# Optimization experiments

Hardware: AMD Instinct MI355X
Metric: run time of the kernel (lower is better)

## Reference

```python
import jax, jax.numpy as jnp
import numpy as np

SINKHORN_ITERS = 100
SINKHORN_EPS = 0.1


def setup_inputs() -> dict:
    key = jax.random.key(0)
    k1, k2 = jax.random.split(key)
    M, N, C = 2048, 2048, 512
    d_M_q = jax.random.normal(k1, (M, C), dtype=jnp.float32)
    d_N_r = jax.random.normal(k2, (N, C), dtype=jnp.float32)
    # pipeline feeds L2-normalized descriptors (F.normalize(..., p=2, dim=1))
    d_M_q = d_M_q / jnp.linalg.norm(d_M_q, axis=1, keepdims=True)
    d_N_r = d_N_r / jnp.linalg.norm(d_N_r, axis=1, keepdims=True)
    z = jnp.float32(0.5)  # learned bin_score scalar
    return {"d_M_q": d_M_q, "d_N_r": d_N_r, "z": z}


def reference(d_M_q, d_N_r, z):
    M, N = d_M_q.shape[0], d_N_r.shape[0]
    # score matmul: (M, C) x (C, N) -> (M, N)
    score = jnp.einsum('mc,nc->mn', d_M_q, d_N_r)
    # augmented (M+1, N+1): dustbin row/col/corner filled with z
    S_aug = jnp.full((M + 1, N + 1), z, dtype=d_M_q.dtype).at[:M, :N].set(score)
    K0 = jnp.exp(S_aug / SINKHORN_EPS)

    def body(i, K):
        K = K / K.sum(axis=1, keepdims=True)  # row normalize
        K = K / K.sum(axis=0, keepdims=True)  # col normalize
        return K

    P_aug = jax.lax.fori_loop(0, SINKHORN_ITERS, body, K0)
    P = P_aug[:M, :N]
    return P, P_aug
```

## Files before the change

### kernel.cpp

```cpp
#include <hip/hip_runtime.h>
#include <hip/hip_fp16.h>

#define ITERS 100
#define AGENT __HIP_MEMORY_SCOPE_AGENT

union PK { unsigned long long u; struct { float v; unsigned tag; } s; };

#define SLOT 136
#define MSG_ONE (2 * 16 * 16 * SLOT)
#define UV_STRIDE 272

__device__ __forceinline__ float wave_sum(float p) {
    p += __shfl_xor(p, 1, 64);
    p += __shfl_xor(p, 2, 64);
    p += __shfl_xor(p, 4, 64);
    p += __shfl_xor(p, 8, 64);
    p += __shfl_xor(p, 16, 64);
    p += __shfl_xor(p, 32, 64);
    return p;
}

__global__ void __launch_bounds__(256, 1)
sinkhorn_fused(const float* __restrict__ Q, const float* __restrict__ R,
               const float* __restrict__ zp, float* __restrict__ out,
               unsigned long long* __restrict__ ws)
{
    __shared__ __align__(16) char smem[66560];
    float* As = (float*)smem;
    float* Bs = (float*)(smem + 32768);
    char*  TrmB = smem;
    char*  TcmB = smem + 32768;
    float* part = (float*)(smem + 65536);

    const int t  = threadIdx.x;
    const int b  = blockIdx.x;
    const int bi = b >> 4, bj = b & 15;
    const int tx = t & 15, ty = t >> 4;
    const int l  = t & 63, w  = t >> 6;
    const int gi0 = bi * 128, gj0 = bj * 128;

    float acc[8][8];
#pragma unroll
    for (int r = 0; r < 8; r++)
#pragma unroll
        for (int c = 0; c < 8; c++) acc[r][c] = 0.f;

    const int lr = t & 31, lc4 = t >> 5;
    const float* Qb = Q + (size_t)gi0 * 512;
    const float* Rb = R + (size_t)gj0 * 512;

    float4 qa[4], ra[4];
#pragma unroll
    for (int i = 0; i < 4; i++) {
        qa[i] = *(const float4*)(Qb + (size_t)(lr + 32 * i) * 512 + 4 * lc4);
        ra[i] = *(const float4*)(Rb + (size_t)(lr + 32 * i) * 512 + 4 * lc4);
    }
#pragma unroll
    for (int i = 0; i < 4; i++) {
        int row = lr + 32 * i;
        As[(4*lc4+0)*128 + row] = qa[i].x;  As[(4*lc4+1)*128 + row] = qa[i].y;
        As[(4*lc4+2)*128 + row] = qa[i].z;  As[(4*lc4+3)*128 + row] = qa[i].w;
        Bs[(4*lc4+0)*128 + row] = ra[i].x;  Bs[(4*lc4+1)*128 + row] = ra[i].y;
        Bs[(4*lc4+2)*128 + row] = ra[i].z;  Bs[(4*lc4+3)*128 + row] = ra[i].w;
    }
    __syncthreads();

    for (int ks = 0; ks < 16; ks++) {
        if (ks < 15) {
            int k0 = (ks + 1) * 32;
#pragma unroll
            for (int i = 0; i < 4; i++) {
                qa[i] = *(const float4*)(Qb + (size_t)(lr+32*i)*512 + k0 + 4*lc4);
                ra[i] = *(const float4*)(Rb + (size_t)(lr+32*i)*512 + k0 + 4*lc4);
            }
        }
        const float* A = As + (ks & 1) * (32 * 128);
        const float* B = Bs + (ks & 1) * (32 * 128);
#pragma unroll 4
        for (int k = 0; k < 32; k++) {
            float4 a0 = *(const float4*)(A + k*128 + 8*ty);
            float4 a1 = *(const float4*)(A + k*128 + 8*ty + 4);
            float4 b0 = *(const float4*)(B + k*128 + 8*tx);
            float4 b1 = *(const float4*)(B + k*128 + 8*tx + 4);
            float av[8] = {a0.x,a0.y,a0.z,a0.w,a1.x,a1.y,a1.z,a1.w};
            float bv[8] = {b0.x,b0.y,b0.z,b0.w,b1.x,b1.y,b1.z,b1.w};
#pragma unroll
            for (int r = 0; r < 8; r++)
#pragma unroll
                for (int c = 0; c < 8; c++)
                    acc[r][c] = fmaf(av[r], bv[c], acc[r][c]);
        }
        if (ks < 15) {
            __syncthreads();
            float* An = As + ((ks+1) & 1) * (32 * 128);
            float* Bn = Bs + ((ks+1) & 1) * (32 * 128);
#pragma unroll
            for (int i = 0; i < 4; i++) {
                int row = lr + 32 * i;
                An[(4*lc4+0)*128 + row] = qa[i].x;  An[(4*lc4+1)*128 + row] = qa[i].y;
                An[(4*lc4+2)*128 + row] = qa[i].z;  An[(4*lc4+3)*128 + row] = qa[i].w;
                Bn[(4*lc4+0)*128 + row] = ra[i].x;  Bn[(4*lc4+1)*128 + row] = ra[i].y;
                Bn[(4*lc4+2)*128 + row] = ra[i].z;  Bn[(4*lc4+3)*128 + row] = ra[i].w;
            }
            __syncthreads();
        }
    }
    __syncthreads();

    const float E = expf(zp[0] * 10.0f);
#pragma unroll
    for (int r = 0; r < 8; r++)
#pragma unroll
        for (int c = 0; c < 8; c++) acc[r][c] = expf(acc[r][c] * 10.0f);

#pragma unroll
    for (int r = 0; r < 8; r++) {
        int rr = 8 * ty + r;
        unsigned short h[8];
#pragma unroll
        for (int c = 0; c < 8; c++) h[c] = __half_as_ushort(__float2half(acc[r][c]));
        uint4 pk;
        pk.x = h[0] | ((unsigned)h[1] << 16); pk.y = h[2] | ((unsigned)h[3] << 16);
        pk.z = h[4] | ((unsigned)h[5] << 16); pk.w = h[6] | ((unsigned)h[7] << 16);
        *(uint4*)(TrmB + rr * 256 + ((tx ^ (rr & 15)) << 4)) = pk;
    }
#pragma unroll
    for (int c = 0; c < 8; c++) {
        int cc = 8 * tx + c;
        unsigned short h[8];
#pragma unroll
        for (int r = 0; r < 8; r++) h[r] = __half_as_ushort(__float2half(acc[r][c]));
        uint4 pk;
        pk.x = h[0] | ((unsigned)h[1] << 16); pk.y = h[2] | ((unsigned)h[3] << 16);
        pk.z = h[4] | ((unsigned)h[5] << 16); pk.w = h[6] | ((unsigned)h[7] << 16);
        *(uint4*)(TcmB + cc * 256 + ((ty ^ (cc & 15)) << 4)) = pk;
    }

    unsigned long long* rmsg = ws;
    unsigned long long* cmsg = ws + MSG_ONE;
    float* uvb  = (float*)(ws + 2 * MSG_ONE) + b * UV_STRIDE;
    float* ubuf = uvb;
    float* vbuf = uvb + 136;

    if (t < 128)      vbuf[t] = 1.0f;
    else if (t < 130) vbuf[t] = 64.0f;
    float uN = 0.f, vN = 1.0f, vsum = 128.0f, usum = 0.f;
    __syncthreads();

    for (int it = 0; it < ITERS; it++) {
        const int buf = it & 1;
        const unsigned tagw = (unsigned)(it + 1);

        {
            unsigned long long* base = rmsg + (size_t)((buf * 16 + bi) * 16) * SLOT;
            if (t == 128) {
                PK p; p.s.v = vsum; p.s.tag = tagw;
                __hip_atomic_store(base + (size_t)bj * SLOT + 128, p.u, __ATOMIC_RELAXED, AGENT);
            }
            if (t < 128) {
                const char* rp = TrmB + t * 256;
                const float4* v4 = (const float4*)vbuf;
                float racc = 0.f;
#pragma unroll
                for (int c = 0; c < 16; c++) {
                    uint4 kq = *(const uint4*)(rp + ((c ^ (t & 15)) << 4));
                    float4 va = v4[2 * c], vb = v4[2 * c + 1];
                    const __half2* h2 = (const __half2*)&kq;
                    float2 f;
                    f = __half22float2(h2[0]); racc = fmaf(f.x, va.x, fmaf(f.y, va.y, racc));
                    f = __half22float2(h2[1]); racc = fmaf(f.x, va.z, fmaf(f.y, va.w, racc));
                    f = __half22float2(h2[2]); racc = fmaf(f.x, vb.x, fmaf(f.y, vb.y, racc));
                    f = __half22float2(h2[3]); racc = fmaf(f.x, vb.z, fmaf(f.y, vb.w, racc));
                }
                PK p; p.s.v = racc; p.s.tag = tagw;
                __hip_atomic_store(base + (size_t)bj * SLOT + t, p.u, __ATOMIC_RELAXED, AGENT);
            }
            float ssum_v = 0.f;
            {
                const int row  = t & 127;
                const int half = t >> 7;
                bool sdone = (half == 1) || (l >= 16);
                float vsv = 0.f, pacc = 0.f;
                unsigned long long* rb = base + (size_t)(8 * half) * SLOT + row;
                for (;;) {
                    PK m[8];
#pragma unroll
                    for (int s = 0; s < 8; s++)
                        m[s].u = __hip_atomic_load(rb + (size_t)s * SLOT,
                                                   __ATOMIC_RELAXED, AGENT);
                    PK vm; vm.u = 0ull;
                    if (!sdone)
                        vm.u = __hip_atomic_load(base + (size_t)l * SLOT + 128,
                                                 __ATOMIC_RELAXED, AGENT);
                    int cnt = 0; float a = 0.f;
#pragma unroll
                    for (int s = 0; s < 8; s++) {
                        bool ok = (m[s].s.tag == tagw);
                        cnt += ok; a += ok ? m[s].s.v : 0.f;
                    }
                    if (!sdone && vm.s.tag == tagw) { vsv = vm.s.v; sdone = true; }
                    if (cnt == 8 && sdone) { pacc = a; break; }
                    __builtin_amdgcn_s_sleep(1);
                }
                part[t] = pacc;
                ssum_v = wave_sum(l < 16 ? vsv : 0.f);
            }
            __syncthreads();
            if (t < 128) {
                float rsum = part[t] + part[t + 128];
                uN = 1.0f / (E * (ssum_v + vN));
                float ui = 1.0f / (rsum + E * vN);
                ubuf[t] = ui;
                float wsm = wave_sum(ui);
                if (l == 0) ubuf[128 + w] = wsm;
            }
            __syncthreads();
            usum = ubuf[128] + ubuf[129];
        }

        {
            unsigned long long* base = cmsg + (size_t)((buf * 16 + bj) * 16) * SLOT;
            if (t == 128) {
                PK p; p.s.v = usum; p.s.tag = tagw;
                __hip_atomic_store(base + (size_t)bi * SLOT + 128, p.u, __ATOMIC_RELAXED, AGENT);
            }
            if (t < 128) {
                const char* cp = TcmB + t * 256;
                const float4* u4 = (const float4*)ubuf;
                float cacc = 0.f;
#pragma unroll
                for (int c = 0; c < 16; c++) {
                    uint4 kq = *(const uint4*)(cp + ((c ^ (t & 15)) << 4));
                    float4 ua = u4[2 * c], ub = u4[2 * c + 1];
                    const __half2* h2 = (const __half2*)&kq;
                    float2 f;
                    f = __half22float2(h2[0]); cacc = fmaf(f.x, ua.x, fmaf(f.y, ua.y, cacc));
                    f = __half22float2(h2[1]); cacc = fmaf(f.x, ua.z, fmaf(f.y, ua.w, cacc));
                    f = __half22float2(h2[2]); cacc = fmaf(f.x, ub.x, fmaf(f.y, ub.y, cacc));
                    f = __half22float2(h2[3]); cacc = fmaf(f.x, ub.z, fmaf(f.y, ub.w, cacc));
                }
                PK p; p.s.v = cacc; p.s.tag = tagw;
                __hip_atomic_store(base + (size_t)bi * SLOT + t, p.u, __ATOMIC_RELAXED, AGENT);
            }
            float ssum_u = 0.f;
            {
                const int row  = t & 127;
                const int half = t >> 7;
                bool sdone = (l >= 16);
                float usv = 0.f, pacc = 0.f;
                unsigned long long* rb = base + (size_t)(8 * half) * SLOT + row;
                for (;;) {
                    PK m[8];
#pragma unroll
                    for (int s = 0; s < 8; s++)
                        m[s].u = __hip_atomic_load(rb + (size_t)s * SLOT,
                                                   __ATOMIC_RELAXED, AGENT);
                    PK um; um.u = 0ull;
                    if (!sdone)
                        um.u = __hip_atomic_load(base + (size_t)l * SLOT + 128,
                                                 __ATOMIC_RELAXED, AGENT);
                    int cnt = 0; float a = 0.f;
#pragma unroll
                    for (int s = 0; s < 8; s++) {
                        bool ok = (m[s].s.tag == tagw);
                        cnt += ok; a += ok ? m[s].s.v : 0.f;
                    }
                    if (!sdone && um.s.tag == tagw) { usv = um.s.v; sdone = true; }
                    if (cnt == 8 && sdone) { pacc = a; break; }
                    __builtin_amdgcn_s_sleep(1);
                }
                part[t] = pacc;
                ssum_u = wave_sum(l < 16 ? usv : 0.f);
            }
            vN = 1.0f / (E * (ssum_u + uN));
            __syncthreads();
            if (t < 128) {
                float csum = part[t] + part[t + 128];
                float vj = 1.0f / (csum + E * uN);
                vbuf[t] = vj;
                float wsm = wave_sum(vj);
                if (l == 0) vbuf[128 + w] = wsm;
            }
            __syncthreads();
            vsum = vbuf[128] + vbuf[129];
        }
    }

    float* P  = out;
    float* PA = out + (size_t)2048 * 2048;
    float2 vv = *(const float2*)&vbuf[2 * l];
#pragma unroll 2
    for (int rr2 = 0; rr2 < 32; rr2++) {
        int i = 32 * w + rr2;
        float ui = ubuf[i];
        const char* rp = TrmB + i * 256;
        int c = l >> 2;
        __half2 h2 = *(const __half2*)(rp + ((c ^ (i & 15)) << 4) + (l & 3) * 4);
        float2 kf = __half22float2(h2);
        float p0 = ui * kf.x * vv.x;
        float p1 = ui * kf.y * vv.y;
        size_t gi = (size_t)(gi0 + i);
        *(float2*)&P[gi * 2048 + gj0 + 2 * l] = make_float2(p0, p1);
        PA[gi * 2049 + gj0 + 2 * l]     = p0;
        PA[gi * 2049 + gj0 + 2 * l + 1] = p1;
        if (bj == 15 && l == 0) PA[gi * 2049 + 2048] = ui * E * vN;
    }
    if (bi == 15 && w == 0) {
        PA[(size_t)2048 * 2049 + gj0 + 2 * l]     = uN * E * vv.x;
        PA[(size_t)2048 * 2049 + gj0 + 2 * l + 1] = uN * E * vv.y;
        if (bj == 15 && l == 0) PA[(size_t)2048 * 2049 + 2048] = uN * E * vN;
    }
}

extern "C" void kernel_launch(void* const* d_in, const int* in_sizes, int n_in,
                              void* d_out, int out_size, void* d_ws, size_t ws_size,
                              hipStream_t stream)
{
    (void)in_sizes; (void)n_in; (void)out_size; (void)ws_size;
    const float* Q  = (const float*)d_in[0];
    const float* R  = (const float*)d_in[1];
    const float* zp = (const float*)d_in[2];
    float* out = (float*)d_out;
    unsigned long long* ws = (unsigned long long*)d_ws;
    void* args[] = { (void*)&Q, (void*)&R, (void*)&zp, (void*)&out, (void*)&ws };
    hipLaunchCooperativeKernel((const void*)sinkhorn_fused, dim3(256), dim3(256),
                               args, 0, stream);
}
```

Baseline: 847.4 us.

## Repartition Sinkhorn kernel into row/column strips with global scaling-vector exchange

```diff
diff --git a/kernel.cpp b/kernel.cpp
--- a/kernel.cpp
+++ b/kernel.cpp
@@ -5,10 +5,6 @@
 #define AGENT __HIP_MEMORY_SCOPE_AGENT
 
 union PK { unsigned long long u; struct { float v; unsigned tag; } s; };
-
-#define SLOT 136
-#define MSG_ONE (2 * 16 * 16 * SLOT)
-#define UV_STRIDE 272
 
 __device__ __forceinline__ float wave_sum(float p) {
     p += __shfl_xor(p, 1, 64);
@@ -25,291 +21,232 @@
                const float* __restrict__ zp, float* __restrict__ out,
                unsigned long long* __restrict__ ws)
 {
-    __shared__ __align__(16) char smem[66560];
-    float* As = (float*)smem;
-    float* Bs = (float*)(smem + 32768);
-    char*  TrmB = smem;
-    char*  TcmB = smem + 32768;
-    float* part = (float*)(smem + 65536);
-
-    const int t  = threadIdx.x;
-    const int b  = blockIdx.x;
-    const int bi = b >> 4, bj = b & 15;
-    const int tx = t & 15, ty = t >> 4;
-    const int l  = t & 63, w  = t >> 6;
-    const int gi0 = bi * 128, gj0 = bj * 128;
-
-    float acc[8][8];
-#pragma unroll
-    for (int r = 0; r < 8; r++)
-#pragma unroll
-        for (int c = 0; c < 8; c++) acc[r][c] = 0.f;
-
-    const int lr = t & 31, lc4 = t >> 5;
-    const float* Qb = Q + (size_t)gi0 * 512;
-    const float* Rb = R + (size_t)gj0 * 512;
-
-    float4 qa[4], ra[4];
-#pragma unroll
-    for (int i = 0; i < 4; i++) {
-        qa[i] = *(const float4*)(Qb + (size_t)(lr + 32 * i) * 512 + 4 * lc4);
-        ra[i] = *(const float4*)(Rb + (size_t)(lr + 32 * i) * 512 + 4 * lc4);
-    }
-#pragma unroll
-    for (int i = 0; i < 4; i++) {
-        int row = lr + 32 * i;
-        As[(4*lc4+0)*128 + row] = qa[i].x;  As[(4*lc4+1)*128 + row] = qa[i].y;
-        As[(4*lc4+2)*128 + row] = qa[i].z;  As[(4*lc4+3)*128 + row] = qa[i].w;
-        Bs[(4*lc4+0)*128 + row] = ra[i].x;  Bs[(4*lc4+1)*128 + row] = ra[i].y;
-        Bs[(4*lc4+2)*128 + row] = ra[i].z;  Bs[(4*lc4+3)*128 + row] = ra[i].w;
-    }
+    __shared__ __align__(16) char smem[66048];
+    char* KrowB = smem;
+    char* KcolB = smem + 32768;
+    float* red  = (float*)(smem + 65536);
+    float* red2 = (float*)(smem + 65664);
+    float* uown = (float*)(smem + 65680);
+    float* vown = (float*)(smem + 65712);
+
+    const int t = threadIdx.x;
+    const int b = blockIdx.x;
+    const int l = t & 63, w = t >> 6;
+    const float E = expf(zp[0] * 10.0f);
+
+    {
+        float acc[8][8];
+#pragma unroll
+        for (int r = 0; r < 8; r++)
+#pragma unroll
+            for (int c = 0; c < 8; c++) acc[r][c] = 0.f;
+        const float* Qs = Q + (size_t)(8 * b) * 512;
+        const float* Rt = R + (size_t)(8 * t) * 512;
+        for (int k = 0; k < 512; k += 4) {
+            float4 r4[8];
+#pragma unroll
+            for (int c = 0; c < 8; c++) r4[c] = *(const float4*)(Rt + c * 512 + k);
+#pragma unroll
+            for (int r = 0; r < 8; r++) {
+                float4 q = *(const float4*)(Qs + r * 512 + k);
+#pragma unroll
+                for (int c = 0; c < 8; c++)
+                    acc[r][c] = fmaf(q.x, r4[c].x, fmaf(q.y, r4[c].y,
+                                fmaf(q.z, r4[c].z, fmaf(q.w, r4[c].w, acc[r][c]))));
+            }
+        }
+#pragma unroll
+        for (int r = 0; r < 8; r++) {
+            unsigned short h[8];
+#pragma unroll
+            for (int c = 0; c < 8; c++)
+                h[c] = __half_as_ushort(__float2half(expf(acc[r][c] * 10.0f)));
+            uint4 pk;
+            pk.x = h[0] | ((unsigned)h[1] << 16); pk.y = h[2] | ((unsigned)h[3] << 16);
+            pk.z = h[4] | ((unsigned)h[5] << 16); pk.w = h[6] | ((unsigned)h[7] << 16);
+            *(uint4*)(KrowB + r * 4096 + t * 16) = pk;
+        }
+    }
+    {
+        float acc[8][8];
+#pragma unroll
+        for (int c = 0; c < 8; c++)
+#pragma unroll
+            for (int i = 0; i < 8; i++) acc[c][i] = 0.f;
+        const float* Rs = R + (size_t)(8 * b) * 512;
+        const float* Qt = Q + (size_t)(8 * t) * 512;
+        for (int k = 0; k < 512; k += 4) {
+            float4 q4[8];
+#pragma unroll
+            for (int i = 0; i < 8; i++) q4[i] = *(const float4*)(Qt + i * 512 + k);
+#pragma unroll
+            for (int c = 0; c < 8; c++) {
+                float4 r = *(const float4*)(Rs + c * 512 + k);
+#pragma unroll
+                for (int i = 0; i < 8; i++)
+                    acc[c][i] = fmaf(r.x, q4[i].x, fmaf(r.y, q4[i].y,
+                                fmaf(r.z, q4[i].z, fmaf(r.w, q4[i].w, acc[c][i]))));
+            }
+        }
+#pragma unroll
+        for (int c = 0; c < 8; c++) {
+            unsigned short h[8];
+#pragma unroll
+            for (int i = 0; i < 8; i++)
+                h[i] = __half_as_ushort(__float2half(expf(acc[c][i] * 10.0f)));
+            uint4 pk;
+            pk.x = h[0] | ((unsigned)h[1] << 16); pk.y = h[2] | ((unsigned)h[3] << 16);
+            pk.z = h[4] | ((unsigned)h[5] << 16); pk.w = h[6] | ((unsigned)h[7] << 16);
+            *(uint4*)(KcolB + c * 4096 + t * 16) = pk;
+        }
+    }
+
+    unsigned long long* umsg = ws;
+    unsigned long long* vmsg = ws + 2 * 2048;
+
+    float v[8], ug[8];
+#pragma unroll
+    for (int c = 0; c < 8; c++) v[c] = 1.0f;
+    float vN = 1.0f, uN = 0.0f, sv = 2048.0f, su = 0.0f;
     __syncthreads();
 
-    for (int ks = 0; ks < 16; ks++) {
-        if (ks < 15) {
-            int k0 = (ks + 1) * 32;
-#pragma unroll
-            for (int i = 0; i < 4; i++) {
-                qa[i] = *(const float4*)(Qb + (size_t)(lr+32*i)*512 + k0 + 4*lc4);
-                ra[i] = *(const float4*)(Rb + (size_t)(lr+32*i)*512 + k0 + 4*lc4);
-            }
-        }
-        const float* A = As + (ks & 1) * (32 * 128);
-        const float* B = Bs + (ks & 1) * (32 * 128);
-#pragma unroll 4
-        for (int k = 0; k < 32; k++) {
-            float4 a0 = *(const float4*)(A + k*128 + 8*ty);
-            float4 a1 = *(const float4*)(A + k*128 + 8*ty + 4);
-            float4 b0 = *(const float4*)(B + k*128 + 8*tx);
-            float4 b1 = *(const float4*)(B + k*128 + 8*tx + 4);
-            float av[8] = {a0.x,a0.y,a0.z,a0.w,a1.x,a1.y,a1.z,a1.w};
-            float bv[8] = {b0.x,b0.y,b0.z,b0.w,b1.x,b1.y,b1.z,b1.w};
-#pragma unroll
-            for (int r = 0; r < 8; r++)
-#pragma unroll
-                for (int c = 0; c < 8; c++)
-                    acc[r][c] = fmaf(av[r], bv[c], acc[r][c]);
-        }
-        if (ks < 15) {
-            __syncthreads();
-            float* An = As + ((ks+1) & 1) * (32 * 128);
-            float* Bn = Bs + ((ks+1) & 1) * (32 * 128);
-#pragma unroll
-            for (int i = 0; i < 4; i++) {
-                int row = lr + 32 * i;
-                An[(4*lc4+0)*128 + row] = qa[i].x;  An[(4*lc4+1)*128 + row] = qa[i].y;
-                An[(4*lc4+2)*128 + row] = qa[i].z;  An[(4*lc4+3)*128 + row] = qa[i].w;
-                Bn[(4*lc4+0)*128 + row] = ra[i].x;  Bn[(4*lc4+1)*128 + row] = ra[i].y;
-                Bn[(4*lc4+2)*128 + row] = ra[i].z;  Bn[(4*lc4+3)*128 + row] = ra[i].w;
-            }
-            __syncthreads();
-        }
-    }
-    __syncthreads();
-
-    const float E = expf(zp[0] * 10.0f);
-#pragma unroll
-    for (int r = 0; r < 8; r++)
-#pragma unroll
-        for (int c = 0; c < 8; c++) acc[r][c] = expf(acc[r][c] * 10.0f);
-
-#pragma unroll
-    for (int r = 0; r < 8; r++) {
-        int rr = 8 * ty + r;
-        unsigned short h[8];
-#pragma unroll
-        for (int c = 0; c < 8; c++) h[c] = __half_as_ushort(__float2half(acc[r][c]));
-        uint4 pk;
-        pk.x = h[0] | ((unsigned)h[1] << 16); pk.y = h[2] | ((unsigned)h[3] << 16);
-        pk.z = h[4] | ((unsigned)h[5] << 16); pk.w = h[6] | ((unsigned)h[7] << 16);
-        *(uint4*)(TrmB + rr * 256 + ((tx ^ (rr & 15)) << 4)) = pk;
-    }
-#pragma unroll
-    for (int c = 0; c < 8; c++) {
-        int cc = 8 * tx + c;
-        unsigned short h[8];
-#pragma unroll
-        for (int r = 0; r < 8; r++) h[r] = __half_as_ushort(__float2half(acc[r][c]));
-        uint4 pk;
-        pk.x = h[0] | ((unsigned)h[1] << 16); pk.y = h[2] | ((unsigned)h[3] << 16);
-        pk.z = h[4] | ((unsigned)h[5] << 16); pk.w = h[6] | ((unsigned)h[7] << 16);
-        *(uint4*)(TcmB + cc * 256 + ((ty ^ (cc & 15)) << 4)) = pk;
-    }
-
-    unsigned long long* rmsg = ws;
-    unsigned long long* cmsg = ws + MSG_ONE;
-    float* uvb  = (float*)(ws + 2 * MSG_ONE) + b * UV_STRIDE;
-    float* ubuf = uvb;
-    float* vbuf = uvb + 136;
-
-    if (t < 128)      vbuf[t] = 1.0f;
-    else if (t < 130) vbuf[t] = 64.0f;
-    float uN = 0.f, vN = 1.0f, vsum = 128.0f, usum = 0.f;
-    __syncthreads();
-
     for (int it = 0; it < ITERS; it++) {
+        const unsigned tagw = (unsigned)(it + 1);
         const int buf = it & 1;
-        const unsigned tagw = (unsigned)(it + 1);
 
         {
-            unsigned long long* base = rmsg + (size_t)((buf * 16 + bi) * 16) * SLOT;
-            if (t == 128) {
-                PK p; p.s.v = vsum; p.s.tag = tagw;
-                __hip_atomic_store(base + (size_t)bj * SLOT + 128, p.u, __ATOMIC_RELAXED, AGENT);
-            }
-            if (t < 128) {
-                const char* rp = TrmB + t * 256;
-                const float4* v4 = (const float4*)vbuf;
-                float racc = 0.f;
-#pragma unroll
-                for (int c = 0; c < 16; c++) {
-                    uint4 kq = *(const uint4*)(rp + ((c ^ (t & 15)) << 4));
-                    float4 va = v4[2 * c], vb = v4[2 * c + 1];
-                    const __half2* h2 = (const __half2*)&kq;
-                    float2 f;
-                    f = __half22float2(h2[0]); racc = fmaf(f.x, va.x, fmaf(f.y, va.y, racc));
-                    f = __half22float2(h2[1]); racc = fmaf(f.x, va.z, fmaf(f.y, va.w, racc));
-                    f = __half22float2(h2[2]); racc = fmaf(f.x, vb.x, fmaf(f.y, vb.y, racc));
-                    f = __half22float2(h2[3]); racc = fmaf(f.x, vb.z, fmaf(f.y, vb.w, racc));
+            float p[8];
+#pragma unroll
+            for (int r = 0; r < 8; r++) p[r] = 0.f;
+#pragma unroll
+            for (int r = 0; r < 8; r++) {
+                uint4 kq = *(const uint4*)(KrowB + r * 4096 + t * 16);
+                const __half2* h2 = (const __half2*)&kq;
+                float2 f;
+                f = __half22float2(h2[0]); p[r] = fmaf(f.x, v[0], fmaf(f.y, v[1], p[r]));
+                f = __half22float2(h2[1]); p[r] = fmaf(f.x, v[2], fmaf(f.y, v[3], p[r]));
+                f = __half22float2(h2[2]); p[r] = fmaf(f.x, v[4], fmaf(f.y, v[5], p[r]));
+                f = __half22float2(h2[3]); p[r] = fmaf(f.x, v[6], fmaf(f.y, v[7], p[r]));
+            }
+#pragma unroll
+            for (int r = 0; r < 8; r++) p[r] = wave_sum(p[r]);
+            if (l == 0) {
+#pragma unroll
+                for (int r = 0; r < 8; r++) red[w * 8 + r] = p[r];
+            }
+            uN = 1.0f / (E * (sv + vN));
+            __syncthreads();
+            if (t < 8) {
+                float rsum = red[t] + red[8 + t] + red[16 + t] + red[24 + t];
+                float uu = 1.0f / (rsum + E * vN);
+                uown[t] = uu;
+                PK pk; pk.s.v = uu; pk.s.tag = tagw;
+                __hip_atomic_store(umsg + (size_t)buf * 2048 + 8 * b + t, pk.u,
+                                   __ATOMIC_RELAXED, AGENT);
+            }
+            unsigned long long* gb = umsg + (size_t)buf * 2048 + 8 * t;
+            for (;;) {
+                PK m[8];
+#pragma unroll
+                for (int s = 0; s < 8; s++)
+                    m[s].u = __hip_atomic_load(gb + s, __ATOMIC_RELAXED, AGENT);
+                int cnt = 0;
+#pragma unroll
+                for (int s = 0; s < 8; s++) cnt += (m[s].s.tag == tagw);
+                if (cnt == 8) {
+#pragma unroll
+                    for (int s = 0; s < 8; s++) ug[s] = m[s].s.v;
+                    break;
                 }
-                PK p; p.s.v = racc; p.s.tag = tagw;
-                __hip_atomic_store(base + (size_t)bj * SLOT + t, p.u, __ATOMIC_RELAXED, AGENT);
-            }
-            float ssum_v = 0.f;
-            {
-                const int row  = t & 127;
-                const int half = t >> 7;
-                bool sdone = (half == 1) || (l >= 16);
-                float vsv = 0.f, pacc = 0.f;
-                unsigned long long* rb = base + (size_t)(8 * half) * SLOT + row;
-                for (;;) {
-                    PK m[8];
-#pragma unroll
-                    for (int s = 0; s < 8; s++)
-                        m[s].u = __hip_atomic_load(rb + (size_t)s * SLOT,
-                                                   __ATOMIC_RELAXED, AGENT);
-                    PK vm; vm.u = 0ull;
-                    if (!sdone)
-                        vm.u = __hip_atomic_load(base + (size_t)l * SLOT + 128,
-                                                 __ATOMIC_RELAXED, AGENT);
-                    int cnt = 0; float a = 0.f;
-#pragma unroll
-                    for (int s = 0; s < 8; s++) {
-                        bool ok = (m[s].s.tag == tagw);
-                        cnt += ok; a += ok ? m[s].s.v : 0.f;
-                    }
-                    if (!sdone && vm.s.tag == tagw) { vsv = vm.s.v; sdone = true; }
-                    if (cnt == 8 && sdone) { pacc = a; break; }
-                    __builtin_amdgcn_s_sleep(1);
+                __builtin_amdgcn_s_sleep(1);
+            }
+            float sp = ug[0] + ug[1] + ug[2] + ug[3] + ug[4] + ug[5] + ug[6] + ug[7];
+            sp = wave_sum(sp);
+            if (l == 0) red2[w] = sp;
+            __syncthreads();
+            su = red2[0] + red2[1] + red2[2] + red2[3];
+        }
+
+        {
+            float p[8];
+#pragma unroll
+            for (int c = 0; c < 8; c++) p[c] = 0.f;
+#pragma unroll
+            for (int c = 0; c < 8; c++) {
+                uint4 kq = *(const uint4*)(KcolB + c * 4096 + t * 16);
+                const __half2* h2 = (const __half2*)&kq;
+                float2 f;
+                f = __half22float2(h2[0]); p[c] = fmaf(f.x, ug[0], fmaf(f.y, ug[1], p[c]));
+                f = __half22float2(h2[1]); p[c] = fmaf(f.x, ug[2], fmaf(f.y, ug[3], p[c]));
+                f = __half22float2(h2[2]); p[c] = fmaf(f.x, ug[4], fmaf(f.y, ug[5], p[c]));
+                f = __half22float2(h2[3]); p[c] = fmaf(f.x, ug[6], fmaf(f.y, ug[7], p[c]));
+            }
+#pragma unroll
+            for (int c = 0; c < 8; c++) p[c] = wave_sum(p[c]);
+            if (l == 0) {
+#pragma unroll
+                for (int c = 0; c < 8; c++) red[w * 8 + c] = p[c];
+            }
+            const float vNn = 1.0f / (E * (su + uN));
+            __syncthreads();
+            if (t < 8) {
+                float csum = red[t] + red[8 + t] + red[16 + t] + red[24 + t];
+                float vv = 1.0f / (csum + E * uN);
+                vown[t] = vv;
+                PK pk; pk.s.v = vv; pk.s.tag = tagw;
+                __hip_atomic_store(vmsg + (size_t)buf * 2048 + 8 * b + t, pk.u,
+                                   __ATOMIC_RELAXED, AGENT);
+            }
+            unsigned long long* gb = vmsg + (size_t)buf * 2048 + 8 * t;
+            for (;;) {
+                PK m[8];
+#pragma unroll
+                for (int s = 0; s < 8; s++)
+                    m[s].u = __hip_atomic_load(gb + s, __ATOMIC_RELAXED, AGENT);
+                int cnt = 0;
+#pragma unroll
+                for (int s = 0; s < 8; s++) cnt += (m[s].s.tag == tagw);
+                if (cnt == 8) {
+#pragma unroll
+                    for (int s = 0; s < 8; s++) v[s] = m[s].s.v;
+                    break;
                 }
-                part[t] = pacc;
-                ssum_v = wave_sum(l < 16 ? vsv : 0.f);
-            }
-            __syncthreads();
-            if (t < 128) {
-                float rsum = part[t] + part[t + 128];
-                uN = 1.0f / (E * (ssum_v + vN));
-                float ui = 1.0f / (rsum + E * vN);
-                ubuf[t] = ui;
-                float wsm = wave_sum(ui);
-                if (l == 0) ubuf[128 + w] = wsm;
-            }
-            __syncthreads();
-            usum = ubuf[128] + ubuf[129];
-        }
-
-        {
-            unsigned long long* base = cmsg + (size_t)((buf * 16 + bj) * 16) * SLOT;
-            if (t == 128) {
-                PK p; p.s.v = usum; p.s.tag = tagw;
-                __hip_atomic_store(base + (size_t)bi * SLOT + 128, p.u, __ATOMIC_RELAXED, AGENT);
-            }
-            if (t < 128) {
-                const char* cp = TcmB + t * 256;
-                const float4* u4 = (const float4*)ubuf;
-                float cacc = 0.f;
-#pragma unroll
-                for (int c = 0; c < 16; c++) {
-                    uint4 kq = *(const uint4*)(cp + ((c ^ (t & 15)) << 4));
-                    float4 ua = u4[2 * c], ub = u4[2 * c + 1];
-                    const __half2* h2 = (const __half2*)&kq;
-                    float2 f;
-                    f = __half22float2(h2[0]); cacc = fmaf(f.x, ua.x, fmaf(f.y, ua.y, cacc));
-                    f = __half22float2(h2[1]); cacc = fmaf(f.x, ua.z, fmaf(f.y, ua.w, cacc));
-                    f = __half22float2(h2[2]); cacc = fmaf(f.x, ub.x, fmaf(f.y, ub.y, cacc));
-                    f = __half22float2(h2[3]); cacc = fmaf(f.x, ub.z, fmaf(f.y, ub.w, cacc));
-                }
-                PK p; p.s.v = cacc; p.s.tag = tagw;
-                __hip_atomic_store(base + (size_t)bi * SLOT + t, p.u, __ATOMIC_RELAXED, AGENT);
-            }
-            float ssum_u = 0.f;
-            {
-                const int row  = t & 127;
-                const int half = t >> 7;
-                bool sdone = (l >= 16);
-                float usv = 0.f, pacc = 0.f;
-                unsigned long long* rb = base + (size_t)(8 * half) * SLOT + row;
-                for (;;) {
-                    PK m[8];
-#pragma unroll
-                    for (int s = 0; s < 8; s++)
-                        m[s].u = __hip_atomic_load(rb + (size_t)s * SLOT,
-                                                   __ATOMIC_RELAXED, AGENT);
-                    PK um; um.u = 0ull;
-                    if (!sdone)
-                        um.u = __hip_atomic_load(base + (size_t)l * SLOT + 128,
-                                                 __ATOMIC_RELAXED, AGENT);
-                    int cnt = 0; float a = 0.f;
-#pragma unroll
-                    for (int s = 0; s < 8; s++) {
-                        bool ok = (m[s].s.tag == tagw);
-                        cnt += ok; a += ok ? m[s].s.v : 0.f;
-                    }
-                    if (!sdone && um.s.tag == tagw) { usv = um.s.v; sdone = true; }
-                    if (cnt == 8 && sdone) { pacc = a; break; }
-                    __builtin_amdgcn_s_sleep(1);
-                }
-                part[t] = pacc;
-                ssum_u = wave_sum(l < 16 ? usv : 0.f);
-            }
-            vN = 1.0f / (E * (ssum_u + uN));
-            __syncthreads();
-            if (t < 128) {
-                float csum = part[t] + part[t + 128];
-                float vj = 1.0f / (csum + E * uN);
-                vbuf[t] = vj;
-                float wsm = wave_sum(vj);
-                if (l == 0) vbuf[128 + w] = wsm;
-            }
-            __syncthreads();
-            vsum = vbuf[128] + vbuf[129];
+                __builtin_amdgcn_s_sleep(1);
+            }
+            float sp = v[0] + v[1] + v[2] + v[3] + v[4] + v[5] + v[6] + v[7];
+            sp = wave_sum(sp);
+            if (l == 0) red2[w] = sp;
+            __syncthreads();
+            sv = red2[0] + red2[1] + red2[2] + red2[3];
+            vN = vNn;
         }
     }
 
     float* P  = out;
     float* PA = out + (size_t)2048 * 2048;
-    float2 vv = *(const float2*)&vbuf[2 * l];
-#pragma unroll 2
-    for (int rr2 = 0; rr2 < 32; rr2++) {
-        int i = 32 * w + rr2;
-        float ui = ubuf[i];
-        const char* rp = TrmB + i * 256;
-        int c = l >> 2;
-        __half2 h2 = *(const __half2*)(rp + ((c ^ (i & 15)) << 4) + (l & 3) * 4);
-        float2 kf = __half22float2(h2);
-        float p0 = ui * kf.x * vv.x;
-        float p1 = ui * kf.y * vv.y;
-        size_t gi = (size_t)(gi0 + i);
-        *(float2*)&P[gi * 2048 + gj0 + 2 * l] = make_float2(p0, p1);
-        PA[gi * 2049 + gj0 + 2 * l]     = p0;
-        PA[gi * 2049 + gj0 + 2 * l + 1] = p1;
-        if (bj == 15 && l == 0) PA[gi * 2049 + 2048] = ui * E * vN;
-    }
-    if (bi == 15 && w == 0) {
-        PA[(size_t)2048 * 2049 + gj0 + 2 * l]     = uN * E * vv.x;
-        PA[(size_t)2048 * 2049 + gj0 + 2 * l + 1] = uN * E * vv.y;
-        if (bj == 15 && l == 0) PA[(size_t)2048 * 2049 + 2048] = uN * E * vN;
-    }
+#pragma unroll
+    for (int r = 0; r < 8; r++) {
+        float ur = uown[r];
+        uint4 kq = *(const uint4*)(KrowB + r * 4096 + t * 16);
+        const __half2* h2 = (const __half2*)&kq;
+        float pv[8];
+        float2 f;
+        f = __half22float2(h2[0]); pv[0] = ur * f.x * v[0]; pv[1] = ur * f.y * v[1];
+        f = __half22float2(h2[1]); pv[2] = ur * f.x * v[2]; pv[3] = ur * f.y * v[3];
+        f = __half22float2(h2[2]); pv[4] = ur * f.x * v[4]; pv[5] = ur * f.y * v[5];
+        f = __half22float2(h2[3]); pv[6] = ur * f.x * v[6]; pv[7] = ur * f.y * v[7];
+        size_t gi = (size_t)(8 * b + r);
+        *(float4*)&P[gi * 2048 + 8 * t]     = make_float4(pv[0], pv[1], pv[2], pv[3]);
+        *(float4*)&P[gi * 2048 + 8 * t + 4] = make_float4(pv[4], pv[5], pv[6], pv[7]);
+        float* pa = &PA[gi * 2049 + 8 * t];
+#pragma unroll
+        for (int c = 0; c < 8; c++) pa[c] = pv[c];
+        if (t == 0) PA[gi * 2049 + 2048] = ur * E * vN;
+    }
+    if (t < 8)
+        PA[(size_t)2048 * 2049 + 8 * b + t] = uN * E * vown[t];
+    if (b == 255 && t == 0)
+        PA[(size_t)2048 * 2049 + 2048] = uN * E * vN;
 }
 
 extern "C" void kernel_launch(void* const* d_in, const int* in_sizes, int n_in,
```

New measurement: 1.649 ms. 94.6% more time.
